# Optimization experiments

Hardware: AMD Instinct MI355X
Metric: run time of the kernel (lower is better)

The kernel has to match this reference:

```python
import jax, jax.numpy as jnp
import numpy as np

EMBED_DIM = 1024
FFN_DIM = 4096
N_QUBITS = 10


def setup_inputs() -> dict:
    key = jax.random.key(0)
    k_x, k_phi, k_w1, k_w2 = jax.random.split(key, 4)
    x = jax.random.normal(k_x, (8, 2048, EMBED_DIM), dtype=jnp.float32)
    # trainable RY angles, one per wire (torchquantum init ~ U(0, 2pi); any init works for a reference)
    ry_params = jax.random.uniform(k_phi, (N_QUBITS,), dtype=jnp.float32, minval=0.0, maxval=2.0 * np.pi)
    # nn.Linear(n_qubits, ffn_dim, bias=False): weight [ffn_dim, n_qubits]
    w1 = jax.random.normal(k_w1, (FFN_DIM, N_QUBITS), dtype=jnp.float32) / np.sqrt(N_QUBITS)
    # nn.Linear(ffn_dim, embed_dim, bias=False): weight [embed_dim, ffn_dim]
    w2 = jax.random.normal(k_w2, (EMBED_DIM, FFN_DIM), dtype=jnp.float32) / np.sqrt(FFN_DIM)
    return {"x": x, "ry_params": ry_params, "w1": w1, "w2": w2}


def reference(x, ry_params, w1, w2):
    # Quantum layer in closed form: wires are unentangled.
    # |0> --RX(x_i)--RY(phi_i)--> <Z_i> = cos(x_i) * cos(phi_i)
    # Only the first N_QUBITS features of each token are encoded.
    q_out = jnp.cos(x[..., :N_QUBITS]) * jnp.cos(ry_params)  # [B, S, nq]
    # dropout is identity in eval mode
    h = jnp.einsum('bsq,fq->bsf', q_out, w1)  # [B, S, ffn]
    h = jax.nn.relu(h)
    return jnp.einsum('bsf,ef->bse', h, w2)  # [B, S, embed]
```

## Files before the change

kernel.cpp:

```cpp
#include <hip/hip_runtime.h>
#include <hip/hip_bf16.h>
#include <stdint.h>

#define M_TOK   16384
#define EMBED   1024
#define FFN     4096
#define NQ      10

typedef __attribute__((ext_vector_type(8))) short  bf16x8;
typedef __attribute__((ext_vector_type(4))) float  f32x4;
typedef __attribute__((ext_vector_type(8))) unsigned short u16x8;

static __device__ __forceinline__ unsigned short f2bf(float f) {
    union { float f; unsigned u; } v; v.f = f;
    unsigned r = v.u + 0x7FFF + ((v.u >> 16) & 1);
    return (unsigned short)(r >> 16);
}

__global__ __launch_bounds__(256) void compute_h(
    const float* __restrict__ x, const float* __restrict__ ry,
    const float* __restrict__ w1, unsigned short* __restrict__ h)
{
    __shared__ float cq[32 * 16];
    __shared__ float cry[NQ];

    const int tid = threadIdx.x;
    const int t0  = blockIdx.x * 32;
    const int fb  = blockIdx.y * 2048 + tid * 8;

    if (tid < NQ) cry[tid] = cosf(ry[tid]);
    for (int idx = tid; idx < 32 * NQ; idx += 256) {
        int t = idx / NQ;
        int i = idx - t * NQ;
        cq[t * 16 + i] = cosf(x[(size_t)(t0 + t) * EMBED + i]);
    }
    __syncthreads();

    float wf[8][NQ];
#pragma unroll
    for (int fi = 0; fi < 8; ++fi)
#pragma unroll
        for (int i = 0; i < NQ; ++i)
            wf[fi][i] = w1[(fb + fi) * NQ + i] * cry[i];

    for (int t = 0; t < 32; ++t) {
        const float4 c0 = *(const float4*)&cq[t * 16 + 0];
        const float4 c1 = *(const float4*)&cq[t * 16 + 4];
        const float2 c2 = *(const float2*)&cq[t * 16 + 8];
        u16x8 v;
#pragma unroll
        for (int fi = 0; fi < 8; ++fi) {
            float s = c0.x * wf[fi][0] + c0.y * wf[fi][1] + c0.z * wf[fi][2]
                    + c0.w * wf[fi][3] + c1.x * wf[fi][4] + c1.y * wf[fi][5]
                    + c1.z * wf[fi][6] + c1.w * wf[fi][7] + c2.x * wf[fi][8]
                    + c2.y * wf[fi][9];
            v[fi] = f2bf(fmaxf(s, 0.f));
        }
        *(u16x8*)(h + (size_t)(t0 + t) * FFN + fb) = v;
    }
}

__global__ __launch_bounds__(256) void conv_w2(
    const float* __restrict__ w2, unsigned short* __restrict__ o)
{
    const int idx = (blockIdx.x * 256 + threadIdx.x) * 8;
    float4 a = *(const float4*)(w2 + idx);
    float4 b = *(const float4*)(w2 + idx + 4);
    u16x8 v;
    v[0] = f2bf(a.x); v[1] = f2bf(a.y); v[2] = f2bf(a.z); v[3] = f2bf(a.w);
    v[4] = f2bf(b.x); v[5] = f2bf(b.y); v[6] = f2bf(b.z); v[7] = f2bf(b.w);
    *(u16x8*)(o + idx) = v;
}

#define GK 4096
#define GN 1024
#define BK 64

#define GL2LDS(g, l) \
    __builtin_amdgcn_global_load_lds( \
        (const __attribute__((address_space(1))) void*)(g), \
        (__attribute__((address_space(3))) void*)(l), 16, 0, 0)

__global__ __launch_bounds__(256) void gemm_bt(
    const unsigned short* __restrict__ A,
    const unsigned short* __restrict__ B,
    float* __restrict__ C)
{
    __shared__ unsigned short At[128 * BK];
    __shared__ unsigned short Bt[128 * BK];

    const int tid  = threadIdx.x;
    const int wv   = tid >> 6;
    const int lane = tid & 63;

    const int bid   = blockIdx.x;
    const int group = bid >> 6;
    const int g     = bid & 63;
    const int m_blk = group * 8 + (g & 7);
    const int n_blk = g >> 3;
    const int m0 = m_blk * 128;
    const int n0 = n_blk * 128;

    const int wr = (wv & 1) * 64;
    const int wc = (wv >> 1) * 64;

    f32x4 acc[4][4] = {};

    const int srow  = lane >> 3;
    const int scolb = ((lane & 7) ^ srow) * 16;

    const int rr = lane & 15;
    const int cc = lane >> 4;
    const int f0off = rr * 128 + (((0 * 4 + cc) ^ (rr & 7)) * 16);
    const int f1off = rr * 128 + (((1 * 4 + cc) ^ (rr & 7)) * 16);

    for (int k0 = 0; k0 < GK; k0 += BK) {
#pragma unroll
        for (int j = 0; j < 4; ++j) {
            const int rbase = wv * 32 + j * 8;
            const char* ag = (const char*)A +
                (((size_t)(m0 + rbase + srow) * GK + k0) * 2 + scolb);
            GL2LDS(ag, (char*)At + rbase * 128);
            const char* bg = (const char*)B +
                (((size_t)(n0 + rbase + srow) * GK + k0) * 2 + scolb);
            GL2LDS(bg, (char*)Bt + rbase * 128);
        }
        __syncthreads();

#pragma unroll
        for (int s = 0; s < 2; ++s) {
            const int foff = s ? f1off : f0off;
            bf16x8 af[4], bf[4];
#pragma unroll
            for (int i = 0; i < 4; ++i) {
                af[i] = *(const bf16x8*)((const char*)At + (wr + i * 16) * 128 + foff);
                bf[i] = *(const bf16x8*)((const char*)Bt + (wc + i * 16) * 128 + foff);
            }
#pragma unroll
            for (int i = 0; i < 4; ++i)
#pragma unroll
                for (int j = 0; j < 4; ++j)
                    acc[i][j] = __builtin_amdgcn_mfma_f32_16x16x32_bf16(
                        af[i], bf[j], acc[i][j], 0, 0, 0);
        }
        __syncthreads();
    }

    const int cn    = lane & 15;
    const int rbase = (lane >> 4) * 4;
#pragma unroll
    for (int i = 0; i < 4; ++i)
#pragma unroll
        for (int j = 0; j < 4; ++j)
#pragma unroll
            for (int r = 0; r < 4; ++r) {
                const int m = m0 + wr + i * 16 + rbase + r;
                const int n = n0 + wc + j * 16 + cn;
                C[(size_t)m * GN + n] = acc[i][j][r];
            }
}

extern "C" void kernel_launch(void* const* d_in, const int* in_sizes, int n_in,
                              void* d_out, int out_size, void* d_ws, size_t ws_size,
                              hipStream_t stream) {
    const float* x  = (const float*)d_in[0];
    const float* ry = (const float*)d_in[1];
    const float* w1 = (const float*)d_in[2];
    const float* w2 = (const float*)d_in[3];
    float* out = (float*)d_out;

    unsigned short* h   = (unsigned short*)d_ws;
    unsigned short* w2b = (unsigned short*)((char*)d_ws +
                           (size_t)M_TOK * FFN * sizeof(unsigned short));

    compute_h<<<dim3(512, 2), 256, 0, stream>>>(x, ry, w1, h);
    conv_w2<<<dim3((EMBED * FFN) / (256 * 8)), 256, 0, stream>>>(w2, w2b);
    gemm_bt<<<dim3(1024), 256, 0, stream>>>(h, w2b, out);
}
```

Before: 293.0 us.

## Add producer wavefront with double-buffered LDS prefetch in bf16 GEMM

Splits the GEMM block into four MFMA consumer waves and one extra producer wave, which streams the next K-tile of A and B into a second LDS buffer. Consumers compute on the current buffer, so global-to-LDS loads of step k+1 can overlap the MFMAs of step k. The point is to hide global load latency that the single-buffered version exposed at every barrier. The cost is doubled LDS use per block, which may lower occupancy, plus one idle-compute wave per block.

```diff
diff --git a/kernel.cpp b/kernel.cpp
--- a/kernel.cpp
+++ b/kernel.cpp
@@ -75,19 +75,20 @@
 #define GK 4096
 #define GN 1024
 #define BK 64
+#define NKI (GK / BK)
 
 #define GL2LDS(g, l) \
     __builtin_amdgcn_global_load_lds( \
         (const __attribute__((address_space(1))) void*)(g), \
         (__attribute__((address_space(3))) void*)(l), 16, 0, 0)
 
-__global__ __launch_bounds__(256) void gemm_bt(
+__global__ __launch_bounds__(320) void gemm_bt(
     const unsigned short* __restrict__ A,
     const unsigned short* __restrict__ B,
     float* __restrict__ C)
 {
-    __shared__ unsigned short At[128 * BK];
-    __shared__ unsigned short Bt[128 * BK];
+    __shared__ unsigned short At[2][128 * BK];
+    __shared__ unsigned short Bt[2][128 * BK];
 
     const int tid  = threadIdx.x;
     const int wv   = tid >> 6;
@@ -101,63 +102,81 @@
     const int m0 = m_blk * 128;
     const int n0 = n_blk * 128;
 
-    const int wr = (wv & 1) * 64;
-    const int wc = (wv >> 1) * 64;
+    if (wv == 4) {
+        const int srow  = lane >> 3;
+        const int scolb = ((lane & 7) ^ srow) * 16;
 
-    f32x4 acc[4][4] = {};
+        const char* Abase = (const char*)A + (size_t)(m0 + srow) * (GK * 2) + scolb;
+        const char* Bbase = (const char*)B + (size_t)(n0 + srow) * (GK * 2) + scolb;
 
-    const int srow  = lane >> 3;
-    const int scolb = ((lane & 7) ^ srow) * 16;
-
-    const int rr = lane & 15;
-    const int cc = lane >> 4;
-    const int f0off = rr * 128 + (((0 * 4 + cc) ^ (rr & 7)) * 16);
-    const int f1off = rr * 128 + (((1 * 4 + cc) ^ (rr & 7)) * 16);
-
-    for (int k0 = 0; k0 < GK; k0 += BK) {
 #pragma unroll
-        for (int j = 0; j < 4; ++j) {
-            const int rbase = wv * 32 + j * 8;
-            const char* ag = (const char*)A +
-                (((size_t)(m0 + rbase + srow) * GK + k0) * 2 + scolb);
-            GL2LDS(ag, (char*)At + rbase * 128);
-            const char* bg = (const char*)B +
-                (((size_t)(n0 + rbase + srow) * GK + k0) * 2 + scolb);
-            GL2LDS(bg, (char*)Bt + rbase * 128);
+        for (int rg = 0; rg < 16; ++rg) {
+            GL2LDS(Abase + (size_t)rg * 8 * (GK * 2), (char*)At[0] + rg * 1024);
+            GL2LDS(Bbase + (size_t)rg * 8 * (GK * 2), (char*)Bt[0] + rg * 1024);
         }
         __syncthreads();
 
+        for (int k = 0; k < NKI; ++k) {
+            if (k + 1 < NKI) {
+                const int s  = (k + 1) & 1;
+                const size_t koff = (size_t)(k + 1) * BK * 2;
 #pragma unroll
-        for (int s = 0; s < 2; ++s) {
-            const int foff = s ? f1off : f0off;
-            bf16x8 af[4], bf[4];
+                for (int rg = 0; rg < 16; ++rg) {
+                    GL2LDS(Abase + (size_t)rg * 8 * (GK * 2) + koff,
+                           (char*)At[s] + rg * 1024);
+                    GL2LDS(Bbase + (size_t)rg * 8 * (GK * 2) + koff,
+                           (char*)Bt[s] + rg * 1024);
+                }
+            }
+            __syncthreads();
+        }
+    } else {
+        const int wr = (wv & 1) * 64;
+        const int wc = (wv >> 1) * 64;
+
+        f32x4 acc[4][4] = {};
+
+        const int rr = lane & 15;
+        const int cc = lane >> 4;
+        const int f0off = rr * 128 + (((0 * 4 + cc) ^ (rr & 7)) * 16);
+        const int f1off = rr * 128 + (((1 * 4 + cc) ^ (rr & 7)) * 16);
+
+        __syncthreads();
+
+        for (int k = 0; k < NKI; ++k) {
+            const int s = k & 1;
 #pragma unroll
-            for (int i = 0; i < 4; ++i) {
-                af[i] = *(const bf16x8*)((const char*)At + (wr + i * 16) * 128 + foff);
-                bf[i] = *(const bf16x8*)((const char*)Bt + (wc + i * 16) * 128 + foff);
+            for (int st = 0; st < 2; ++st) {
+                const int foff = st ? f1off : f0off;
+                bf16x8 af[4], bf[4];
+#pragma unroll
+                for (int i = 0; i < 4; ++i) {
+                    af[i] = *(const bf16x8*)((const char*)At[s] + (wr + i * 16) * 128 + foff);
+                    bf[i] = *(const bf16x8*)((const char*)Bt[s] + (wc + i * 16) * 128 + foff);
+                }
+#pragma unroll
+                for (int i = 0; i < 4; ++i)
+#pragma unroll
+                    for (int j = 0; j < 4; ++j)
+                        acc[i][j] = __builtin_amdgcn_mfma_f32_16x16x32_bf16(
+                            af[i], bf[j], acc[i][j], 0, 0, 0);
             }
+            __syncthreads();
+        }
+
+        const int cn    = lane & 15;
+        const int rbase = (lane >> 4) * 4;
 #pragma unroll
-            for (int i = 0; i < 4; ++i)
+        for (int i = 0; i < 4; ++i)
 #pragma unroll
-                for (int j = 0; j < 4; ++j)
-                    acc[i][j] = __builtin_amdgcn_mfma_f32_16x16x32_bf16(
-                        af[i], bf[j], acc[i][j], 0, 0, 0);
-        }
-        __syncthreads();
+            for (int j = 0; j < 4; ++j)
+#pragma unroll
+                for (int r = 0; r < 4; ++r) {
+                    const int m = m0 + wr + i * 16 + rbase + r;
+                    const int n = n0 + wc + j * 16 + cn;
+                    C[(size_t)m * GN + n] = acc[i][j][r];
+                }
     }
-
-    const int cn    = lane & 15;
-    const int rbase = (lane >> 4) * 4;
-#pragma unroll
-    for (int i = 0; i < 4; ++i)
-#pragma unroll
-        for (int j = 0; j < 4; ++j)
-#pragma unroll
-            for (int r = 0; r < 4; ++r) {
-                const int m = m0 + wr + i * 16 + rbase + r;
-                const int n = n0 + wc + j * 16 + cn;
-                C[(size_t)m * GN + n] = acc[i][j][r];
-            }
 }
 
 extern "C" void kernel_launch(void* const* d_in, const int* in_sizes, int n_in,
@@ -175,5 +194,5 @@
 
     compute_h<<<dim3(512, 2), 256, 0, stream>>>(x, ry, w1, h);
     conv_w2<<<dim3((EMBED * FFN) / (256 * 8)), 256, 0, stream>>>(w2, w2b);
-    gemm_bt<<<dim3(1024), 256, 0, stream>>>(h, w2b, out);
+    gemm_bt<<<dim3(1024), 320, 0, stream>>>(h, w2b, out);
 }
```

Result: slower. 333.6 us (+13.9%).
